# Performance work log

Measured on AMD Instinct MI355X. Metric: run time of the kernel, lower is better.

Reference implementation:

```python
import jax, jax.numpy as jnp
import numpy as np

T = 900   # max_time_steps
H = 400   # num_hidden
C = 73    # num_classes
F = 240   # input feature dim
B = 32    # batch


def _masked_lstm(x, mask, Wx, Wh, b):
    """Keras-semantics masked LSTM, return_sequences=True.

    Gate order i,f,g,o (Keras). At masked steps state and output are carried
    forward unchanged (Keras RNN mask behavior).
    x: [B,T,F], mask: [B,T] bool. Returns [B,T,H].
    """
    xz = jnp.einsum('btf,fg->btg', x, Wx) + b  # [B,T,4H] input projection, hoisted out of scan

    def step(carry, inp):
        h, c = carry
        z_t, m = inp
        z = z_t + h @ Wh                     # [B,4H]
        i, f, g, o = jnp.split(z, 4, axis=-1)
        c_new = jax.nn.sigmoid(f) * c + jax.nn.sigmoid(i) * jnp.tanh(g)
        h_new = jax.nn.sigmoid(o) * jnp.tanh(c_new)
        m = m[:, None]
        h = jnp.where(m, h_new, h)
        c = jnp.where(m, c_new, c)
        return (h, c), h

    b_ = x.shape[0]
    init = (jnp.zeros((b_, H), x.dtype), jnp.zeros((b_, H), x.dtype))
    _, hs = jax.lax.scan(step, init, (jnp.swapaxes(xz, 0, 1), mask.T))
    return jnp.swapaxes(hs, 0, 1)  # [B,T,H]


def setup_inputs() -> dict:
    key = jax.random.key(0)
    ks = jax.random.split(key, 10)

    def g(k, shape):
        return (jax.random.normal(k, shape, jnp.float32) * 0.05)

    # unit_forget_bias=True in Keras LSTM: forget-gate bias initialized to 1
    b_init = jnp.concatenate([jnp.zeros((H,)), jnp.ones((H,)), jnp.zeros((2 * H,))]).astype(jnp.float32)

    return {
        'x': jax.random.normal(ks[0], (B, T, F), jnp.float32),
        'seq_len': jax.random.randint(ks[1], (B,), 1, T + 1),
        'Wx_c': g(ks[2], (F, 4 * H)), 'Wh_c': g(ks[3], (H, 4 * H)), 'b_c': b_init,
        'Wx_l': g(ks[4], (F, 4 * H)), 'Wh_l': g(ks[5], (H, 4 * H)), 'b_l': b_init,
        'Wd_c': g(ks[6], (H, C)), 'bd_c': jnp.zeros((C,), jnp.float32),
        'Wd_l': g(ks[7], (H, C)), 'bd_l': jnp.zeros((C,), jnp.float32),
    }


def reference(x, seq_len, Wx_c, Wh_c, b_c, Wx_l, Wh_l, b_l, Wd_c, bd_c, Wd_l, bd_l):
    mask = jnp.arange(T)[None, :] < seq_len[:, None]   # tf.sequence_mask
    h_cells = _masked_lstm(x, mask, Wx_c, Wh_c, b_c)
    logits_cells = h_cells @ Wd_c + bd_c               # [B,T,C]
    h_lstm = _masked_lstm(x, mask, Wx_l, Wh_l, b_l)
    logits_lstm = h_lstm @ Wd_l + bd_l                 # [B,T,C]
    max_abs_diff = jnp.max(jnp.abs(logits_cells - logits_lstm))
    return logits_cells, logits_lstm, max_abs_diff
```

## Files before the change

### kernel.cpp

```cpp
#include <hip/hip_runtime.h>
#include <math.h>

#define T_N 900
#define H_N 400
#define C_N 73
#define F_N 240
#define B_N 32
#define G4H 1600
#define BT  (B_N * T_N)

#define TC    180
#define NCHUNK (T_N / TC)
#define MROWS (B_N * TC)

#define RG   8
#define NGRP 4
#define NBLK 25
#define HSZ  16
#define KCH  100
#define HELEM (RG * H_N)

#define XZC_OFF 0ULL
#define XZC_SZ  ((size_t)MROWS * G4H)
#define HSC_OFF (XZC_OFF + 2 * XZC_SZ)
#define HSC_SZ  ((size_t)MROWS * H_N)
#define HB_OFF  (HSC_OFF + 2 * HSC_SZ)
#define HB_U64  ((size_t)2 * NGRP * 2 * HELEM)
#define STH_OFF (HB_OFF + 2 * HB_U64)
#define STC_OFF (STH_OFF + 2 * B_N * H_N)
#define WS_TOTAL (STC_OFF + 2 * B_N * H_N)

typedef unsigned long long u64;

__device__ __forceinline__ float sigf(float x) {
    return 1.0f / (1.0f + expf(-x));
}

#define GM_BM 128
#define GM_BN 128
#define GM_BK 16

__global__ __launch_bounds__(256)
void xz_gemm(const float* __restrict__ x,
             const float* __restrict__ Wx_c, const float* __restrict__ b_c,
             const float* __restrict__ Wx_l, const float* __restrict__ b_l,
             float* __restrict__ xzc, int t0)
{
    const int L = blockIdx.z;
    const float* W    = L ? Wx_l : Wx_c;
    const float* bias = L ? b_l  : b_c;
    float* out = xzc + (size_t)L * XZC_SZ;

    const int m0 = blockIdx.y * GM_BM;
    const int n0 = blockIdx.x * GM_BN;
    const int tid = threadIdx.x;

    __shared__ float As[GM_BK][GM_BM + 4];
    __shared__ float Bs[GM_BK][GM_BN + 4];

    const int ty = tid >> 4;
    const int tx = tid & 15;

    float acc[8][8];
#pragma unroll
    for (int i = 0; i < 8; ++i)
#pragma unroll
        for (int j = 0; j < 8; ++j) acc[i][j] = 0.0f;

    const int ar = tid & 127;
    const int aq = (tid >> 7) * 8;
    const int kr = tid >> 5;
    const int bc = (tid & 31) * 4;

    const int mrow = m0 + ar;
    const int bb   = mrow / TC;
    const int ss   = mrow - bb * TC;
    const float* arow = x + ((size_t)bb * T_N + t0 + ss) * F_N;

    for (int k0 = 0; k0 < F_N; k0 += GM_BK) {
        {
            const float* ap = arow + k0 + aq;
            float4 a0 = *(const float4*)ap;
            float4 a1 = *(const float4*)(ap + 4);
            As[aq + 0][ar] = a0.x; As[aq + 1][ar] = a0.y;
            As[aq + 2][ar] = a0.z; As[aq + 3][ar] = a0.w;
            As[aq + 4][ar] = a1.x; As[aq + 5][ar] = a1.y;
            As[aq + 6][ar] = a1.z; As[aq + 7][ar] = a1.w;
        }
#pragma unroll
        for (int kk = kr * 2; kk < kr * 2 + 2; ++kk) {
            const float* wp = W + (size_t)(k0 + kk) * G4H;
#pragma unroll
            for (int q = 0; q < 4; ++q) {
                int gc = n0 + bc + q;
                Bs[kk][bc + q] = (gc < G4H) ? wp[gc] : 0.0f;
            }
        }
        __syncthreads();

#pragma unroll
        for (int kk = 0; kk < GM_BK; ++kk) {
            float a[8], b[8];
            *(float4*)&a[0] = *(const float4*)&As[kk][ty * 8];
            *(float4*)&a[4] = *(const float4*)&As[kk][ty * 8 + 4];
            *(float4*)&b[0] = *(const float4*)&Bs[kk][tx * 8];
            *(float4*)&b[4] = *(const float4*)&Bs[kk][tx * 8 + 4];
#pragma unroll
            for (int i = 0; i < 8; ++i)
#pragma unroll
                for (int j = 0; j < 8; ++j)
                    acc[i][j] = fmaf(a[i], b[j], acc[i][j]);
        }
        __syncthreads();
    }

#pragma unroll
    for (int i = 0; i < 8; ++i) {
        const int m = m0 + ty * 8 + i;
#pragma unroll
        for (int j = 0; j < 8; ++j) {
            const int c = n0 + tx * 8 + j;
            if (c < G4H)
                out[(size_t)m * G4H + c] = acc[i][j] + bias[c];
        }
    }
}

__global__ __launch_bounds__(256)
void lstm_rec(const float* __restrict__ Wh_c, const float* __restrict__ Wh_l,
              const int* __restrict__ seq_len,
              const float* __restrict__ xzc,
              float* __restrict__ hsc,
              u64* __restrict__ hb64,
              float* __restrict__ st_h, float* __restrict__ st_c,
              int t0)
{
    __shared__ float hsm[RG][404];
    __shared__ float part[4][RG][64];

    const int bid = blockIdx.x;
    const int L   = bid / (NGRP * NBLK);
    const int rem = bid % (NGRP * NBLK);
    const int g   = rem / NBLK;
    const int nb  = rem % NBLK;
    const int tid  = threadIdx.x;
    const int wave = tid >> 6;
    const int lane = tid & 63;

    const float* Wh = L ? Wh_l : Wh_c;
    const float* xz = xzc + (size_t)L * XZC_SZ;
    float* hs = hsc + (size_t)L * HSC_SZ;
    u64* hb = hb64 + (size_t)(L * NGRP + g) * (2 * HELEM);

    const int gate = lane >> 4;
    const int jj_l = lane & 15;
    const int gcol = gate * H_N + nb * HSZ + jj_l;
    float wreg[KCH];
    {
        const float* wp = Wh + (size_t)(wave * KCH) * G4H + gcol;
#pragma unroll
        for (int kk = 0; kk < KCH; ++kk) wreg[kk] = wp[(size_t)kk * G4H];
    }

    int maxlen = 0;
#pragma unroll
    for (int r = 0; r < RG; ++r) {
        int v = seq_len[g * RG + r];
        maxlen = v > maxlen ? v : maxlen;
    }

    const int t1 = t0 + TC;
    const int tse = maxlen < t1 ? maxlen : t1;

    const int rr  = tid >> 4;
    const int jjs = tid & 15;
    const int bidx = g * RG + rr;
    const int uu   = nb * HSZ + jjs;
    const int mylen = (tid < 128) ? seq_len[bidx] : 0;
    const int stidx = (L * B_N + bidx) * H_N + uu;
    float cst = 0.0f, hst = 0.0f;
    if (tid < 128 && t0 > 0) {
        hst = st_h[stidx];
        cst = st_c[stidx];
    }

    float xzn[4] = {0.f, 0.f, 0.f, 0.f};
    if (tid < 128 && t0 < tse) {
#pragma unroll
        for (int q = 0; q < 4; ++q)
            xzn[q] = xz[(size_t)bidx * TC * G4H + q * H_N + uu];
    }

    for (int t = t0; t < tse; ++t) {
        const int s = t - t0;

        {
            const u64* src = hb + (size_t)(t & 1) * HELEM;
            u64 vv[13];
#pragma unroll
            for (int i = 0; i < 13; ++i) {
                const int e = tid + (i << 8);
                if (e < HELEM)
                    vv[i] = __hip_atomic_load(src + e, __ATOMIC_RELAXED,
                                              __HIP_MEMORY_SCOPE_AGENT);
            }
#pragma unroll
            for (int i = 0; i < 13; ++i) {
                const int e = tid + (i << 8);
                if (e < HELEM) {
                    u64 xv = vv[i];
                    while ((unsigned)(xv >> 32) != (unsigned)t)
                        xv = __hip_atomic_load(src + e, __ATOMIC_RELAXED,
                                               __HIP_MEMORY_SCOPE_AGENT);
                    const int r = (int)((unsigned)e / 400u);
                    const int k = e - r * 400;
                    hsm[r][k] = __uint_as_float((unsigned)xv);
                }
            }
        }
        __syncthreads();

        float acc[RG];
#pragma unroll
        for (int r = 0; r < RG; ++r) acc[r] = 0.0f;
#pragma unroll
        for (int k4 = 0; k4 < KCH / 4; ++k4) {
            float4 hv[RG];
#pragma unroll
            for (int r = 0; r < RG; ++r)
                hv[r] = *(const float4*)&hsm[r][wave * KCH + k4 * 4];
            float w0 = wreg[k4 * 4 + 0];
            float w1 = wreg[k4 * 4 + 1];
            float w2 = wreg[k4 * 4 + 2];
            float w3 = wreg[k4 * 4 + 3];
#pragma unroll
            for (int r = 0; r < RG; ++r) {
                acc[r] = fmaf(w0, hv[r].x, acc[r]);
                acc[r] = fmaf(w1, hv[r].y, acc[r]);
                acc[r] = fmaf(w2, hv[r].z, acc[r]);
                acc[r] = fmaf(w3, hv[r].w, acc[r]);
            }
        }
#pragma unroll
        for (int r = 0; r < RG; ++r) part[wave][r][lane] = acc[r];
        __syncthreads();

        if (tid < 128) {
            float z[4];
#pragma unroll
            for (int q = 0; q < 4; ++q) {
                const int c = q * HSZ + jjs;
                z[q] = part[0][rr][c] + part[1][rr][c] +
                       part[2][rr][c] + part[3][rr][c] + xzn[q];
            }
            const float iv = sigf(z[0]);
            const float fv = sigf(z[1]);
            const float gv = tanhf(z[2]);
            const float ov = sigf(z[3]);
            if (t < mylen) {
                cst = fv * cst + iv * gv;
                hst = ov * tanhf(cst);
            }
            hs[((size_t)bidx * TC + s) * H_N + uu] = hst;

            const u64 pack = ((u64)(unsigned)(t + 1) << 32) |
                             (u64)__float_as_uint(hst);
            __hip_atomic_store(hb + (size_t)((t + 1) & 1) * HELEM +
                               (rr * H_N + uu),
                               pack, __ATOMIC_RELAXED,
                               __HIP_MEMORY_SCOPE_AGENT);

            if (t + 1 < tse) {
#pragma unroll
                for (int q = 0; q < 4; ++q)
                    xzn[q] = xz[((size_t)bidx * TC + (s + 1)) * G4H + q * H_N + uu];
            }
        }
    }

    if (tid < 128) {
        const int ts = tse > t0 ? tse : t0;
        for (int t = ts; t < t1; ++t) {
            const int s = t - t0;
            hs[((size_t)bidx * TC + s) * H_N + uu] = hst;
        }
        st_h[stidx] = hst;
        st_c[stidx] = cst;
    }
}

__global__ __launch_bounds__(256)
void dense_proj(const float* __restrict__ hsc,
                const float* __restrict__ Wd_c, const float* __restrict__ bd_c,
                const float* __restrict__ Wd_l, const float* __restrict__ bd_l,
                float* __restrict__ out, int t0)
{
    const int L = blockIdx.y;
    const float* hs = hsc + (size_t)L * HSC_SZ;
    const float* Wd = L ? Wd_l : Wd_c;
    const float* bd = L ? bd_l : bd_c;
    float* o = out + (size_t)L * ((size_t)BT * C_N);

    const int m0 = blockIdx.x * 128;
    const int tid = threadIdx.x;

    __shared__ float As[16][132];
    __shared__ float Bs[16][80];

    const int r  = tid >> 1;
    const int kq = (tid & 1) * 8;
    const float* ap_base = hs + (size_t)(m0 + r) * H_N + kq;

    const int ty = tid >> 4, tx = tid & 15;
    float acc[8][5];
#pragma unroll
    for (int i = 0; i < 8; ++i)
#pragma unroll
        for (int j = 0; j < 5; ++j) acc[i][j] = 0.0f;

    for (int k0 = 0; k0 < H_N; k0 += 16) {
        float4 a0 = *(const float4*)(ap_base + k0);
        float4 a1 = *(const float4*)(ap_base + k0 + 4);
        As[kq + 0][r] = a0.x; As[kq + 1][r] = a0.y;
        As[kq + 2][r] = a0.z; As[kq + 3][r] = a0.w;
        As[kq + 4][r] = a1.x; As[kq + 5][r] = a1.y;
        As[kq + 6][r] = a1.z; As[kq + 7][r] = a1.w;
        for (int i = tid; i < 16 * 80; i += 256) {
            int kk = i / 80, c = i - kk * 80;
            Bs[kk][c] = (c < C_N) ? Wd[(size_t)(k0 + kk) * C_N + c] : 0.0f;
        }
        __syncthreads();
#pragma unroll
        for (int kk = 0; kk < 16; ++kk) {
            float a[8], bb[5];
            *(float4*)&a[0] = *(const float4*)&As[kk][ty * 8];
            *(float4*)&a[4] = *(const float4*)&As[kk][ty * 8 + 4];
#pragma unroll
            for (int j = 0; j < 5; ++j) bb[j] = Bs[kk][tx * 5 + j];
#pragma unroll
            for (int i = 0; i < 8; ++i)
#pragma unroll
                for (int j = 0; j < 5; ++j)
                    acc[i][j] = fmaf(a[i], bb[j], acc[i][j]);
        }
        __syncthreads();
    }

#pragma unroll
    for (int i = 0; i < 8; ++i) {
        const int m = m0 + ty * 8 + i;
        const int bb = m / TC;
        const int ssg = m - bb * TC + t0;
        float* orow = o + ((size_t)bb * T_N + ssg) * C_N;
#pragma unroll
        for (int j = 0; j < 5; ++j) {
            const int c = tx * 5 + j;
            if (c < C_N)
                orow[c] = acc[i][j] + bd[c];
        }
    }
}

__global__ void maxdiff_k(const float* __restrict__ a,
                          const float* __restrict__ b,
                          int* __restrict__ outbits, size_t n)
{
    size_t i0 = (size_t)blockIdx.x * blockDim.x + threadIdx.x;
    float m = 0.0f;
    for (size_t i = i0; i < n; i += (size_t)gridDim.x * blockDim.x) {
        float d = fabsf(a[i] - b[i]);
        m = d > m ? d : m;
    }
#pragma unroll
    for (int off = 32; off > 0; off >>= 1) {
        float o = __shfl_down(m, off, 64);
        m = o > m ? o : m;
    }
    __shared__ float sm[4];
    if ((threadIdx.x & 63) == 0) sm[threadIdx.x >> 6] = m;
    __syncthreads();
    if (threadIdx.x == 0) {
        float mm = sm[0];
#pragma unroll
        for (int w = 1; w < 4; ++w) mm = sm[w] > mm ? sm[w] : mm;
        atomicMax(outbits, __float_as_int(mm));
    }
}

extern "C" void kernel_launch(void* const* d_in, const int* in_sizes, int n_in,
                              void* d_out, int out_size, void* d_ws, size_t ws_size,
                              hipStream_t stream)
{
    const float* x    = (const float*)d_in[0];
    const int*   slen = (const int*)  d_in[1];
    const float* Wx_c = (const float*)d_in[2];
    const float* Wh_c = (const float*)d_in[3];
    const float* b_c  = (const float*)d_in[4];
    const float* Wx_l = (const float*)d_in[5];
    const float* Wh_l = (const float*)d_in[6];
    const float* b_l  = (const float*)d_in[7];
    const float* Wd_c = (const float*)d_in[8];
    const float* bd_c = (const float*)d_in[9];
    const float* Wd_l = (const float*)d_in[10];
    const float* bd_l = (const float*)d_in[11];

    float* ws    = (float*)d_ws;
    float* xzbuf = ws + XZC_OFF;
    float* hsbuf = ws + HSC_OFF;
    u64*   hb64  = (u64*)(ws + HB_OFF);
    float* st_h  = ws + STH_OFF;
    float* st_c  = ws + STC_OFF;
    float* out   = (float*)d_out;

    hipMemsetAsync(hb64, 0, HB_U64 * sizeof(u64), stream);
    hipMemsetAsync(out + 2 * (size_t)BT * C_N, 0, sizeof(float), stream);

    for (int chunk = 0; chunk < NCHUNK; ++chunk) {
        const int t0 = chunk * TC;

        {
            dim3 grid((G4H + GM_BN - 1) / GM_BN, MROWS / GM_BM, 2);
            xz_gemm<<<grid, 256, 0, stream>>>(x, Wx_c, b_c, Wx_l, b_l,
                                              xzbuf, t0);
        }
        {
            lstm_rec<<<dim3(2 * NGRP * NBLK), dim3(256), 0, stream>>>(
                Wh_c, Wh_l, slen, xzbuf, hsbuf, hb64, st_h, st_c, t0);
        }
        {
            dim3 grid(MROWS / 128, 2);
            dense_proj<<<grid, 256, 0, stream>>>(hsbuf, Wd_c, bd_c,
                                                 Wd_l, bd_l, out, t0);
        }
    }

    maxdiff_k<<<dim3(1024), 256, 0, stream>>>(
        out, out + (size_t)BT * C_N, (int*)(out + 2 * (size_t)BT * C_N),
        (size_t)BT * C_N);
}
```

Measured before the change: 7.811 ms.

## Fuse input projection into persistent recurrent kernel and drop time chunking

Removes the separate xz GEMM and the five-chunk launch loop. The recurrent kernel now keeps a slice of Wx in registers and computes each step's input projection itself, prefetching the next step's x into shared memory while it waits on the h exchange. The h polling loop is rewritten so each wave loads only its own K slice with retry flags, and one __syncthreads per step is removed. This cuts global traffic and launch overhead for the xz buffer, in exchange for about 160 more registers per thread (launch_bounds 256,1) and more serial per-step compute on the critical path.

Measured after the change: 12.57 ms. 61.0% more time.

```diff
diff --git a/kernel.cpp b/kernel.cpp
--- a/kernel.cpp
+++ b/kernel.cpp
@@ -9,26 +9,18 @@
 #define G4H 1600
 #define BT  (B_N * T_N)
 
-#define TC    180
-#define NCHUNK (T_N / TC)
-#define MROWS (B_N * TC)
-
 #define RG   8
 #define NGRP 4
 #define NBLK 25
 #define HSZ  16
 #define KCH  100
+#define KXC  60
 #define HELEM (RG * H_N)
 
-#define XZC_OFF 0ULL
-#define XZC_SZ  ((size_t)MROWS * G4H)
-#define HSC_OFF (XZC_OFF + 2 * XZC_SZ)
-#define HSC_SZ  ((size_t)MROWS * H_N)
-#define HB_OFF  (HSC_OFF + 2 * HSC_SZ)
+#define HS_OFF  0ULL
+#define HS_SZ   ((size_t)BT * H_N)
+#define HB_OFF  (2 * HS_SZ)
 #define HB_U64  ((size_t)2 * NGRP * 2 * HELEM)
-#define STH_OFF (HB_OFF + 2 * HB_U64)
-#define STC_OFF (STH_OFF + 2 * B_N * H_N)
-#define WS_TOTAL (STC_OFF + 2 * B_N * H_N)
 
 typedef unsigned long long u64;
 
@@ -36,106 +28,17 @@
     return 1.0f / (1.0f + expf(-x));
 }
 
-#define GM_BM 128
-#define GM_BN 128
-#define GM_BK 16
-
-__global__ __launch_bounds__(256)
-void xz_gemm(const float* __restrict__ x,
-             const float* __restrict__ Wx_c, const float* __restrict__ b_c,
-             const float* __restrict__ Wx_l, const float* __restrict__ b_l,
-             float* __restrict__ xzc, int t0)
-{
-    const int L = blockIdx.z;
-    const float* W    = L ? Wx_l : Wx_c;
-    const float* bias = L ? b_l  : b_c;
-    float* out = xzc + (size_t)L * XZC_SZ;
-
-    const int m0 = blockIdx.y * GM_BM;
-    const int n0 = blockIdx.x * GM_BN;
-    const int tid = threadIdx.x;
-
-    __shared__ float As[GM_BK][GM_BM + 4];
-    __shared__ float Bs[GM_BK][GM_BN + 4];
-
-    const int ty = tid >> 4;
-    const int tx = tid & 15;
-
-    float acc[8][8];
-#pragma unroll
-    for (int i = 0; i < 8; ++i)
-#pragma unroll
-        for (int j = 0; j < 8; ++j) acc[i][j] = 0.0f;
-
-    const int ar = tid & 127;
-    const int aq = (tid >> 7) * 8;
-    const int kr = tid >> 5;
-    const int bc = (tid & 31) * 4;
-
-    const int mrow = m0 + ar;
-    const int bb   = mrow / TC;
-    const int ss   = mrow - bb * TC;
-    const float* arow = x + ((size_t)bb * T_N + t0 + ss) * F_N;
-
-    for (int k0 = 0; k0 < F_N; k0 += GM_BK) {
-        {
-            const float* ap = arow + k0 + aq;
-            float4 a0 = *(const float4*)ap;
-            float4 a1 = *(const float4*)(ap + 4);
-            As[aq + 0][ar] = a0.x; As[aq + 1][ar] = a0.y;
-            As[aq + 2][ar] = a0.z; As[aq + 3][ar] = a0.w;
-            As[aq + 4][ar] = a1.x; As[aq + 5][ar] = a1.y;
-            As[aq + 6][ar] = a1.z; As[aq + 7][ar] = a1.w;
-        }
-#pragma unroll
-        for (int kk = kr * 2; kk < kr * 2 + 2; ++kk) {
-            const float* wp = W + (size_t)(k0 + kk) * G4H;
-#pragma unroll
-            for (int q = 0; q < 4; ++q) {
-                int gc = n0 + bc + q;
-                Bs[kk][bc + q] = (gc < G4H) ? wp[gc] : 0.0f;
-            }
-        }
-        __syncthreads();
-
-#pragma unroll
-        for (int kk = 0; kk < GM_BK; ++kk) {
-            float a[8], b[8];
-            *(float4*)&a[0] = *(const float4*)&As[kk][ty * 8];
-            *(float4*)&a[4] = *(const float4*)&As[kk][ty * 8 + 4];
-            *(float4*)&b[0] = *(const float4*)&Bs[kk][tx * 8];
-            *(float4*)&b[4] = *(const float4*)&Bs[kk][tx * 8 + 4];
-#pragma unroll
-            for (int i = 0; i < 8; ++i)
-#pragma unroll
-                for (int j = 0; j < 8; ++j)
-                    acc[i][j] = fmaf(a[i], b[j], acc[i][j]);
-        }
-        __syncthreads();
-    }
-
-#pragma unroll
-    for (int i = 0; i < 8; ++i) {
-        const int m = m0 + ty * 8 + i;
-#pragma unroll
-        for (int j = 0; j < 8; ++j) {
-            const int c = n0 + tx * 8 + j;
-            if (c < G4H)
-                out[(size_t)m * G4H + c] = acc[i][j] + bias[c];
-        }
-    }
-}
-
-__global__ __launch_bounds__(256)
+__global__ __launch_bounds__(256, 1)
 void lstm_rec(const float* __restrict__ Wh_c, const float* __restrict__ Wh_l,
+              const float* __restrict__ Wx_c, const float* __restrict__ Wx_l,
+              const float* __restrict__ b_c,  const float* __restrict__ b_l,
               const int* __restrict__ seq_len,
-              const float* __restrict__ xzc,
-              float* __restrict__ hsc,
-              u64* __restrict__ hb64,
-              float* __restrict__ st_h, float* __restrict__ st_c,
-              int t0)
+              const float* __restrict__ x,
+              float* __restrict__ hs_all,
+              u64* __restrict__ hb64)
 {
     __shared__ float hsm[RG][404];
+    __shared__ float xsm[RG][244];
     __shared__ float part[4][RG][64];
 
     const int bid = blockIdx.x;
@@ -148,19 +51,25 @@
     const int lane = tid & 63;
 
     const float* Wh = L ? Wh_l : Wh_c;
-    const float* xz = xzc + (size_t)L * XZC_SZ;
-    float* hs = hsc + (size_t)L * HSC_SZ;
+    const float* Wx = L ? Wx_l : Wx_c;
+    const float* bv = L ? b_l  : b_c;
+    float* hs = hs_all + (size_t)L * HS_SZ;
     u64* hb = hb64 + (size_t)(L * NGRP + g) * (2 * HELEM);
+
+    float* hsm_f = &hsm[0][0];
+    float* xsm_f = &xsm[0][0];
 
     const int gate = lane >> 4;
     const int jj_l = lane & 15;
     const int gcol = gate * H_N + nb * HSZ + jj_l;
     float wreg[KCH];
-    {
-        const float* wp = Wh + (size_t)(wave * KCH) * G4H + gcol;
-#pragma unroll
-        for (int kk = 0; kk < KCH; ++kk) wreg[kk] = wp[(size_t)kk * G4H];
-    }
+#pragma unroll
+    for (int kk = 0; kk < KCH; ++kk)
+        wreg[kk] = Wh[(size_t)(wave * KCH + kk) * G4H + gcol];
+    float wxreg[KXC];
+#pragma unroll
+    for (int kk = 0; kk < KXC; ++kk)
+        wxreg[kk] = Wx[(size_t)(wave * KXC + kk) * G4H + gcol];
 
     int maxlen = 0;
 #pragma unroll
@@ -169,76 +78,126 @@
         maxlen = v > maxlen ? v : maxlen;
     }
 
-    const int t1 = t0 + TC;
-    const int tse = maxlen < t1 ? maxlen : t1;
+    int ea[13], lofs[13];
+#pragma unroll
+    for (int i = 0; i < 13; ++i) {
+        const int j = lane + (i << 6);
+        const int r = j / 100;
+        const int k = wave * KCH + (j - r * 100);
+        ea[i]   = (j < 800) ? (r * H_N + k) : -1;
+        lofs[i] = r * 404 + k;
+    }
+    int xgofs[8], xlofs[8];
+#pragma unroll
+    for (int i = 0; i < 8; ++i) {
+        const int j2 = lane + (i << 6);
+        const int r = j2 / 60;
+        const int kx = wave * KXC + (j2 - r * 60);
+        xgofs[i] = (j2 < 480) ? (int)((g * RG + r) * (T_N * F_N) + kx) : -1;
+        xlofs[i] = r * 244 + kx;
+    }
 
     const int rr  = tid >> 4;
     const int jjs = tid & 15;
     const int bidx = g * RG + rr;
     const int uu   = nb * HSZ + jjs;
     const int mylen = (tid < 128) ? seq_len[bidx] : 0;
-    const int stidx = (L * B_N + bidx) * H_N + uu;
+    float bq[4] = {0.f, 0.f, 0.f, 0.f};
+    if (tid < 128) {
+#pragma unroll
+        for (int q = 0; q < 4; ++q) bq[q] = bv[q * H_N + uu];
+    }
     float cst = 0.0f, hst = 0.0f;
-    if (tid < 128 && t0 > 0) {
-        hst = st_h[stidx];
-        cst = st_c[stidx];
-    }
-
-    float xzn[4] = {0.f, 0.f, 0.f, 0.f};
-    if (tid < 128 && t0 < tse) {
-#pragma unroll
-        for (int q = 0; q < 4; ++q)
-            xzn[q] = xz[(size_t)bidx * TC * G4H + q * H_N + uu];
-    }
-
-    for (int t = t0; t < tse; ++t) {
-        const int s = t - t0;
+
+    float accx[RG];
+#pragma unroll
+    for (int r = 0; r < RG; ++r) accx[r] = 0.0f;
+    if (maxlen > 0) {
+        float xr[8];
+#pragma unroll
+        for (int i = 0; i < 8; ++i)
+            if (xgofs[i] >= 0) xr[i] = x[xgofs[i]];
+#pragma unroll
+        for (int i = 0; i < 8; ++i)
+            if (xgofs[i] >= 0) xsm_f[xlofs[i]] = xr[i];
+#pragma unroll
+        for (int k4 = 0; k4 < KXC / 4; ++k4) {
+            const float w0 = wxreg[k4 * 4 + 0];
+            const float w1 = wxreg[k4 * 4 + 1];
+            const float w2 = wxreg[k4 * 4 + 2];
+            const float w3 = wxreg[k4 * 4 + 3];
+#pragma unroll
+            for (int r = 0; r < RG; ++r) {
+                const float4 xv = *(const float4*)&xsm[r][wave * KXC + k4 * 4];
+                accx[r] = fmaf(w0, xv.x, accx[r]);
+                accx[r] = fmaf(w1, xv.y, accx[r]);
+                accx[r] = fmaf(w2, xv.z, accx[r]);
+                accx[r] = fmaf(w3, xv.w, accx[r]);
+            }
+        }
+    }
+
+    for (int t = 0; t < maxlen; ++t) {
+        const int tn = t + 1;
+        const bool ldx = (tn < maxlen);
+
+        float xr[8];
+        if (ldx) {
+#pragma unroll
+            for (int i = 0; i < 8; ++i)
+                if (xgofs[i] >= 0) xr[i] = x[xgofs[i] + tn * F_N];
+        }
 
         {
             const u64* src = hb + (size_t)(t & 1) * HELEM;
-            u64 vv[13];
-#pragma unroll
-            for (int i = 0; i < 13; ++i) {
-                const int e = tid + (i << 8);
-                if (e < HELEM)
-                    vv[i] = __hip_atomic_load(src + e, __ATOMIC_RELAXED,
-                                              __HIP_MEMORY_SCOPE_AGENT);
-            }
-#pragma unroll
-            for (int i = 0; i < 13; ++i) {
-                const int e = tid + (i << 8);
-                if (e < HELEM) {
-                    u64 xv = vv[i];
-                    while ((unsigned)(xv >> 32) != (unsigned)t)
-                        xv = __hip_atomic_load(src + e, __ATOMIC_RELAXED,
-                                               __HIP_MEMORY_SCOPE_AGENT);
-                    const int r = (int)((unsigned)e / 400u);
-                    const int k = e - r * 400;
-                    hsm[r][k] = __uint_as_float((unsigned)xv);
+            u64 v[13];
+            bool rdy[13];
+#pragma unroll
+            for (int i = 0; i < 13; ++i) rdy[i] = (ea[i] < 0);
+            bool pend = true;
+            while (pend) {
+                pend = false;
+#pragma unroll
+                for (int i = 0; i < 13; ++i)
+                    if (!rdy[i])
+                        v[i] = __hip_atomic_load(src + ea[i], __ATOMIC_RELAXED,
+                                                 __HIP_MEMORY_SCOPE_AGENT);
+#pragma unroll
+                for (int i = 0; i < 13; ++i) {
+                    if (!rdy[i]) {
+                        if ((unsigned)(v[i] >> 32) == (unsigned)t) {
+                            hsm_f[lofs[i]] = __uint_as_float((unsigned)v[i]);
+                            rdy[i] = true;
+                        } else {
+                            pend = true;
+                        }
+                    }
                 }
             }
         }
-        __syncthreads();
+
+        if (ldx) {
+#pragma unroll
+            for (int i = 0; i < 8; ++i)
+                if (xgofs[i] >= 0) xsm_f[xlofs[i]] = xr[i];
+        }
 
         float acc[RG];
 #pragma unroll
-        for (int r = 0; r < RG; ++r) acc[r] = 0.0f;
+        for (int r = 0; r < RG; ++r) acc[r] = accx[r];
 #pragma unroll
         for (int k4 = 0; k4 < KCH / 4; ++k4) {
-            float4 hv[RG];
-#pragma unroll
-            for (int r = 0; r < RG; ++r)
-                hv[r] = *(const float4*)&hsm[r][wave * KCH + k4 * 4];
-            float w0 = wreg[k4 * 4 + 0];
-            float w1 = wreg[k4 * 4 + 1];
-            float w2 = wreg[k4 * 4 + 2];
-            float w3 = wreg[k4 * 4 + 3];
+            const float w0 = wreg[k4 * 4 + 0];
+            const float w1 = wreg[k4 * 4 + 1];
+            const float w2 = wreg[k4 * 4 + 2];
+            const float w3 = wreg[k4 * 4 + 3];
 #pragma unroll
             for (int r = 0; r < RG; ++r) {
-                acc[r] = fmaf(w0, hv[r].x, acc[r]);
-                acc[r] = fmaf(w1, hv[r].y, acc[r]);
-                acc[r] = fmaf(w2, hv[r].z, acc[r]);
-                acc[r] = fmaf(w3, hv[r].w, acc[r]);
+                const float4 hv = *(const float4*)&hsm[r][wave * KCH + k4 * 4];
+                acc[r] = fmaf(w0, hv.x, acc[r]);
+                acc[r] = fmaf(w1, hv.y, acc[r]);
+                acc[r] = fmaf(w2, hv.z, acc[r]);
+                acc[r] = fmaf(w3, hv.w, acc[r]);
             }
         }
 #pragma unroll
@@ -251,7 +210,7 @@
             for (int q = 0; q < 4; ++q) {
                 const int c = q * HSZ + jjs;
                 z[q] = part[0][rr][c] + part[1][rr][c] +
-                       part[2][rr][c] + part[3][rr][c] + xzn[q];
+                       part[2][rr][c] + part[3][rr][c] + bq[q];
             }
             const float iv = sigf(z[0]);
             const float fv = sigf(z[1]);
@@ -261,42 +220,50 @@
                 cst = fv * cst + iv * gv;
                 hst = ov * tanhf(cst);
             }
-            hs[((size_t)bidx * TC + s) * H_N + uu] = hst;
-
-            const u64 pack = ((u64)(unsigned)(t + 1) << 32) |
+            const u64 pack = ((u64)(unsigned)tn << 32) |
                              (u64)__float_as_uint(hst);
-            __hip_atomic_store(hb + (size_t)((t + 1) & 1) * HELEM +
-                               (rr * H_N + uu),
+            __hip_atomic_store(hb + (size_t)(tn & 1) * HELEM + (rr * H_N + uu),
                                pack, __ATOMIC_RELAXED,
                                __HIP_MEMORY_SCOPE_AGENT);
-
-            if (t + 1 < tse) {
-#pragma unroll
-                for (int q = 0; q < 4; ++q)
-                    xzn[q] = xz[((size_t)bidx * TC + (s + 1)) * G4H + q * H_N + uu];
+            hs[((size_t)bidx * T_N + t) * H_N + uu] = hst;
+        }
+        __syncthreads();
+
+        if (ldx) {
+#pragma unroll
+            for (int r = 0; r < RG; ++r) accx[r] = 0.0f;
+#pragma unroll
+            for (int k4 = 0; k4 < KXC / 4; ++k4) {
+                const float w0 = wxreg[k4 * 4 + 0];
+                const float w1 = wxreg[k4 * 4 + 1];
+                const float w2 = wxreg[k4 * 4 + 2];
+                const float w3 = wxreg[k4 * 4 + 3];
+#pragma unroll
+                for (int r = 0; r < RG; ++r) {
+                    const float4 xv = *(const float4*)&xsm[r][wave * KXC + k4 * 4];
+                    accx[r] = fmaf(w0, xv.x, accx[r]);
+                    accx[r] = fmaf(w1, xv.y, accx[r]);
+                    accx[r] = fmaf(w2, xv.z, accx[r]);
+                    accx[r] = fmaf(w3, xv.w, accx[r]);
+                }
             }
         }
     }
 
     if (tid < 128) {
-        const int ts = tse > t0 ? tse : t0;
-        for (int t = ts; t < t1; ++t) {
-            const int s = t - t0;
-            hs[((size_t)bidx * TC + s) * H_N + uu] = hst;
-        }
-        st_h[stidx] = hst;
-        st_c[stidx] = cst;
+        for (int t = maxlen; t < T_N; ++t)
+            hs[((size_t)bidx * T_N + t) * H_N + uu] = hst;
     }
 }
 
 __global__ __launch_bounds__(256)
-void dense_proj(const float* __restrict__ hsc,
+void dense_proj(const float* __restrict__ hs_all,
                 const float* __restrict__ Wd_c, const float* __restrict__ bd_c,
                 const float* __restrict__ Wd_l, const float* __restrict__ bd_l,
-                float* __restrict__ out, int t0)
+                float* __restrict__ out)
 {
     const int L = blockIdx.y;
-    const float* hs = hsc + (size_t)L * HSC_SZ;
+    const float* hs = hs_all + (size_t)L * HS_SZ;
     const float* Wd = L ? Wd_l : Wd_c;
     const float* bd = L ? bd_l : bd_c;
     float* o = out + (size_t)L * ((size_t)BT * C_N);
@@ -349,14 +316,11 @@
 #pragma unroll
     for (int i = 0; i < 8; ++i) {
         const int m = m0 + ty * 8 + i;
-        const int bb = m / TC;
-        const int ssg = m - bb * TC + t0;
-        float* orow = o + ((size_t)bb * T_N + ssg) * C_N;
 #pragma unroll
         for (int j = 0; j < 5; ++j) {
             const int c = tx * 5 + j;
             if (c < C_N)
-                orow[c] = acc[i][j] + bd[c];
+                o[(size_t)m * C_N + c] = acc[i][j] + bd[c];
         }
     }
 }
@@ -405,33 +369,20 @@
     const float* bd_l = (const float*)d_in[11];
 
     float* ws    = (float*)d_ws;
-    float* xzbuf = ws + XZC_OFF;
-    float* hsbuf = ws + HSC_OFF;
+    float* hsbuf = ws + HS_OFF;
     u64*   hb64  = (u64*)(ws + HB_OFF);
-    float* st_h  = ws + STH_OFF;
-    float* st_c  = ws + STC_OFF;
     float* out   = (float*)d_out;
 
     hipMemsetAsync(hb64, 0, HB_U64 * sizeof(u64), stream);
     hipMemsetAsync(out + 2 * (size_t)BT * C_N, 0, sizeof(float), stream);
 
-    for (int chunk = 0; chunk < NCHUNK; ++chunk) {
-        const int t0 = chunk * TC;
-
-        {
-            dim3 grid((G4H + GM_BN - 1) / GM_BN, MROWS / GM_BM, 2);
-            xz_gemm<<<grid, 256, 0, stream>>>(x, Wx_c, b_c, Wx_l, b_l,
-                                              xzbuf, t0);
-        }
-        {
-            lstm_rec<<<dim3(2 * NGRP * NBLK), dim3(256), 0, stream>>>(
-                Wh_c, Wh_l, slen, xzbuf, hsbuf, hb64, st_h, st_c, t0);
-        }
-        {
-            dim3 grid(MROWS / 128, 2);
-            dense_proj<<<grid, 256, 0, stream>>>(hsbuf, Wd_c, bd_c,
-                                                 Wd_l, bd_l, out, t0);
-        }
+    lstm_rec<<<dim3(2 * NGRP * NBLK), dim3(256), 0, stream>>>(
+        Wh_c, Wh_l, Wx_c, Wx_l, b_c, b_l, slen, x, hsbuf, hb64);
+
+    {
+        dim3 grid(BT / 128, 2);
+        dense_proj<<<grid, 256, 0, stream>>>(hsbuf, Wd_c, bd_c, Wd_l, bd_l,
+                                             out);
     }
 
     maxdiff_k<<<dim3(1024), 256, 0, stream>>>(
```
